# Optimization experiments

Measured on AMD Instinct MI355X. Metric: run time of the kernel, lower is better.

## Reference

```python
import jax, jax.numpy as jnp
import numpy as np

B, S, H, R, NH = 4, 2048, 1024, 512, 8
HD = R // NH
EPS = 1e-5


def _ln(x, g, b):
    m = jnp.mean(x, axis=-1, keepdims=True)
    v = jnp.mean(jnp.square(x - m), axis=-1, keepdims=True)
    return (x - m) * jax.lax.rsqrt(v + EPS) * g + b


def setup_inputs() -> dict:
    key = jax.random.key(0)
    ks = iter(jax.random.split(key, 40))
    s = 0.02
    d = {}
    d['hidden_states'] = jax.random.normal(next(ks), (B, S, H), dtype=jnp.float32)
    # complexity assessor: H -> H//4 -> 32 -> 1
    d['ca_w1'] = jax.random.normal(next(ks), (H, H // 4)) * s
    d['ca_b1'] = jnp.zeros((H // 4,))
    d['ca_w2'] = jax.random.normal(next(ks), (H // 4, 32)) * s
    d['ca_b2'] = jnp.zeros((32,))
    d['ca_w3'] = jax.random.normal(next(ks), (32, 1)) * s
    d['ca_b3'] = jnp.zeros((1,))
    # reasoning projection H -> R, and pre-norm
    d['rp_w'] = jax.random.normal(next(ks), (H, R)) * s
    d['rp_b'] = jnp.zeros((R,))
    d['rn_g'] = jnp.ones((R,)); d['rn_b'] = jnp.zeros((R,))
    # transformer encoder layer (norm_first)
    d['ln1_g'] = jnp.ones((R,)); d['ln1_b'] = jnp.zeros((R,))
    d['wqkv'] = jax.random.normal(next(ks), (R, 3 * R)) * s
    d['bqkv'] = jnp.zeros((3 * R,))
    d['wo'] = jax.random.normal(next(ks), (R, R)) * s
    d['bo'] = jnp.zeros((R,))
    d['ln2_g'] = jnp.ones((R,)); d['ln2_b'] = jnp.zeros((R,))
    d['ff1_w'] = jax.random.normal(next(ks), (R, 4 * R)) * s
    d['ff1_b'] = jnp.zeros((4 * R,))
    d['ff2_w'] = jax.random.normal(next(ks), (4 * R, R)) * s
    d['ff2_b'] = jnp.zeros((R,))
    # output projection R -> H and norm
    d['op_w'] = jax.random.normal(next(ks), (R, H)) * s
    d['op_b'] = jnp.zeros((H,))
    d['on_g'] = jnp.ones((H,)); d['on_b'] = jnp.zeros((H,))
    # integration gate: 2H -> H -> H
    d['gw1'] = jax.random.normal(next(ks), (2 * H, H)) * s
    d['gb1'] = jnp.zeros((H,))
    d['gw2'] = jax.random.normal(next(ks), (H, H)) * s
    d['gb2'] = jnp.zeros((H,))
    return d


def reference(hidden_states, ca_w1, ca_b1, ca_w2, ca_b2, ca_w3, ca_b3,
              rp_w, rp_b, rn_g, rn_b, ln1_g, ln1_b, wqkv, bqkv, wo, bo,
              ln2_g, ln2_b, ff1_w, ff1_b, ff2_w, ff2_b, op_w, op_b,
              on_g, on_b, gw1, gb1, gw2, gb2):
    # complexity assessment (metrics only; input_ids=None forces reasoning on all)
    pooled = jnp.mean(hidden_states, axis=1)  # [B,H]
    h = jax.nn.relu(pooled @ ca_w1 + ca_b1)
    h = jax.nn.relu(h @ ca_w2 + ca_b2)
    complexity_scores = jax.nn.sigmoid(h @ ca_w3 + ca_b3)[:, 0]  # [B]

    # apply_reasoning on full batch (should_reason is all-True)
    r = _ln(hidden_states @ rp_w + rp_b, rn_g, rn_b)  # [B,S,R]

    # TransformerEncoderLayer, norm_first, relu, dropout=0
    y = _ln(r, ln1_g, ln1_b)
    qkv = y @ wqkv + bqkv
    q, k, v = jnp.split(qkv, 3, axis=-1)
    q = q.reshape(B, S, NH, HD)
    k = k.reshape(B, S, NH, HD)
    v = v.reshape(B, S, NH, HD)
    scores = jnp.einsum('bqhd,bkhd->bhqk', q, k) / np.sqrt(HD).astype(np.float32)
    attn = jax.nn.softmax(scores, axis=-1)
    o = jnp.einsum('bhqk,bkhd->bqhd', attn, v).reshape(B, S, R)
    r = r + (o @ wo + bo)
    y = _ln(r, ln2_g, ln2_b)
    r = r + (jax.nn.relu(y @ ff1_w + ff1_b) @ ff2_w + ff2_b)

    reasoned = _ln(r @ op_w + op_b, on_g, on_b)  # [B,S,H]

    # sigmoid integration gate on concat([states, reasoned])
    gate_in = jnp.concatenate([hidden_states, reasoned], axis=-1)
    g = jax.nn.relu(gate_in @ gw1 + gb1)
    g = jax.nn.sigmoid(g @ gw2 + gb2)
    output = hidden_states + g * reasoned
    return output, complexity_scores
```

## Files before the change

### kernel.cpp

```cpp
#include <hip/hip_runtime.h>
#include <hip/hip_bf16.h>
#include <math.h>


typedef __bf16 bf16;
typedef __attribute__((ext_vector_type(8))) __bf16 bf16x8;
typedef __attribute__((ext_vector_type(4))) float f32x4;
typedef __attribute__((ext_vector_type(16))) float f32x16;

__device__ __forceinline__ void glds16(const bf16* g, bf16* l) {
  __builtin_amdgcn_global_load_lds(
      (const __attribute__((address_space(1))) void*)g,
      (__attribute__((address_space(3))) void*)l, 16, 0, 0);
}

struct TD { const float* src; char* dst; int rows, cols, tx, start, outbf; };
struct TDs { TD d[9]; };
__global__ void k_trans_all(TDs td) {
  int bid = blockIdx.x;
  int si = 0;
  for (int i = 1; i < 9; i++)
    if (bid >= td.d[i].start) si = i;
  TD dd = td.d[si];
  int tid = bid - dd.start;
  int bx = tid % dd.tx, by = tid / dd.tx;
  __shared__ float tile[32][33];
  int c0 = bx * 32, r0 = by * 32;
  int tx = threadIdx.x, ty = threadIdx.y;
  for (int i = 0; i < 32; i += 8)
    tile[ty + i][tx] = dd.src[(long)(r0 + ty + i) * dd.cols + (c0 + tx)];
  __syncthreads();
  if (dd.outbf) {
    bf16* o = (bf16*)dd.dst;
    for (int i = 0; i < 32; i += 8)
      o[(long)(c0 + ty + i) * dd.rows + (r0 + tx)] = (bf16)tile[tx][ty + i];
  } else {
    float* o = (float*)dd.dst;
    for (int i = 0; i < 32; i += 8)
      o[(long)(c0 + ty + i) * dd.rows + (r0 + tx)] = tile[tx][ty + i];
  }
}

__global__ void k_cvt(const float* __restrict__ in, bf16* __restrict__ out) {
  long i = ((long)blockIdx.x * 256 + threadIdx.x) * 4;
  float4 v = *(const float4*)(in + i);
  bf16* o = out + i;
  o[0] = (bf16)v.x; o[1] = (bf16)v.y; o[2] = (bf16)v.z; o[3] = (bf16)v.w;
}

__global__ void k_vtrans(const bf16* __restrict__ qkv, bf16* __restrict__ VT) {
  __shared__ bf16 tile[32][33];
  int bh = blockIdx.z, b = bh >> 3, h = bh & 7;
  const bf16* in = qkv + (long)b * 2048 * 1536 + 1024 + h * 64;
  bf16* out = VT + (long)bh * 64 * 2048;
  int c0 = blockIdx.x * 32, r0 = blockIdx.y * 32;
  int tx = threadIdx.x, ty = threadIdx.y;
  for (int i = 0; i < 32; i += 8)
    tile[ty + i][tx] = in[(long)(r0 + ty + i) * 1536 + (c0 + tx)];
  __syncthreads();
  for (int i = 0; i < 32; i += 8)
    out[(long)(c0 + ty + i) * 2048 + (r0 + tx)] = tile[tx][ty + i];
}

__global__ void k_pool_part(const float* __restrict__ X, float* __restrict__ part) {
  int b = blockIdx.y, c = blockIdx.z;
  int col = blockIdx.x * 256 + threadIdx.x;
  const float* p = X + (long)b * 2048 * 1024 + (long)c * 128 * 1024 + col;
  float s = 0.f;
  for (int i = 0; i < 128; i++) s += p[(long)i * 1024];
  part[((long)c * 4 + b) * 1024 + col] = s;
}

__global__ void k_pool_fin(const float* __restrict__ part, float* __restrict__ pooled) {
  int idx = blockIdx.x * 256 + threadIdx.x;
  int b = idx >> 10, col = idx & 1023;
  float s = 0.f;
  for (int c = 0; c < 16; c++) s += part[((long)c * 4 + b) * 1024 + col];
  pooled[idx] = s * (1.0f / 2048.0f);
}

__global__ void k_ca1(const float* __restrict__ pooled, const float* __restrict__ w1T,
                      const float* __restrict__ b1, float* __restrict__ h1) {
  int t = blockIdx.x, b = threadIdx.x >> 6, lane = threadIdx.x & 63;
  const float* wr = w1T + (long)t * 1024 + lane * 16;
  const float* pr = pooled + b * 1024 + lane * 16;
  float acc = 0.f;
  for (int j = 0; j < 4; j++) {
    float4 w = *(const float4*)(wr + j * 4);
    float4 p = *(const float4*)(pr + j * 4);
    acc += w.x * p.x + w.y * p.y + w.z * p.z + w.w * p.w;
  }
  for (int off = 32; off; off >>= 1) acc += __shfl_xor(acc, off);
  if (lane == 0) h1[b * 256 + t] = fmaxf(acc + b1[t], 0.f);
}

__global__ void k_ca2(const float* __restrict__ h1,
                      const float* __restrict__ w2, const float* __restrict__ b2,
                      const float* __restrict__ w3, const float* __restrict__ b3,
                      float* __restrict__ scores) {
  __shared__ float w2s[256 * 32];
  __shared__ float h1s[4 * 256];
  __shared__ float h2s[4][32];
  int t = threadIdx.x;
  for (int j = 0; j < 32; j++) w2s[j * 256 + t] = w2[j * 256 + t];
  for (int j = 0; j < 4; j++) h1s[j * 256 + t] = h1[j * 256 + t];
  __syncthreads();
  if (t < 128) {
    int b = t >> 5, o = t & 31;
    float acc = b2[o];
    for (int k = 0; k < 256; k++) acc += h1s[b * 256 + k] * w2s[k * 32 + o];
    h2s[b][o] = fmaxf(acc, 0.f);
  }
  __syncthreads();
  if (t < 4) {
    float acc = b3[0];
    for (int k = 0; k < 32; k++) acc += h2s[t][k] * w3[k];
    scores[t] = 1.f / (1.f + expf(-acc));
  }
}

template <int NCOL>
__global__ void k_ln(const bf16* __restrict__ in, const float* __restrict__ g,
                     const float* __restrict__ be, bf16* __restrict__ out) {
  int wave = threadIdx.x >> 6, lane = threadIdx.x & 63;
  long row = (long)blockIdx.x * 4 + wave;
  const bf16* x = in + row * NCOL;
  constexpr int PER = NCOL / 64;
  constexpr int CH = PER / 8;
  float v[PER];
  float s = 0.f;
  for (int c = 0; c < CH; c++) {
    bf16x8 t = *(const bf16x8*)(x + c * 512 + lane * 8);
    for (int j = 0; j < 8; j++) { v[c * 8 + j] = (float)t[j]; s += v[c * 8 + j]; }
  }
  for (int off = 32; off; off >>= 1) s += __shfl_xor(s, off);
  float mean = s * (1.0f / NCOL);
  float q = 0.f;
  for (int i = 0; i < PER; i++) { float d = v[i] - mean; q += d * d; }
  for (int off = 32; off; off >>= 1) q += __shfl_xor(q, off);
  float rstd = rsqrtf(q * (1.0f / NCOL) + 1e-5f);
  for (int c = 0; c < CH; c++) {
    bf16x8 o;
    for (int j = 0; j < 8; j++) {
      int col = c * 512 + lane * 8 + j;
      o[j] = (bf16)((v[c * 8 + j] - mean) * rstd * g[col] + be[col]);
    }
    *(bf16x8*)(out + row * NCOL + c * 512 + lane * 8) = o;
  }
}

__global__ void k_ln2(const bf16* __restrict__ in,
                      const float* __restrict__ g1, const float* __restrict__ b1,
                      const float* __restrict__ g2, const float* __restrict__ b2,
                      bf16* __restrict__ outR, bf16* __restrict__ outY) {
  int wave = threadIdx.x >> 6, lane = threadIdx.x & 63;
  long row = (long)blockIdx.x * 4 + wave;
  const bf16* x = in + row * 512;
  float v[8];
  float s = 0.f;
  bf16x8 t = *(const bf16x8*)(x + lane * 8);
  for (int j = 0; j < 8; j++) { v[j] = (float)t[j]; s += v[j]; }
  for (int off = 32; off; off >>= 1) s += __shfl_xor(s, off);
  float mean = s * (1.0f / 512);
  float q = 0.f;
  for (int j = 0; j < 8; j++) { float d = v[j] - mean; q += d * d; }
  for (int off = 32; off; off >>= 1) q += __shfl_xor(q, off);
  float rstd = rsqrtf(q * (1.0f / 512) + 1e-5f);
  float r[8];
  float s2 = 0.f;
  bf16x8 orr;
  for (int j = 0; j < 8; j++) {
    int col = lane * 8 + j;
    r[j] = (v[j] - mean) * rstd * g1[col] + b1[col];
    orr[j] = (bf16)r[j];
    s2 += r[j];
  }
  *(bf16x8*)(outR + row * 512 + lane * 8) = orr;
  for (int off = 32; off; off >>= 1) s2 += __shfl_xor(s2, off);
  float mean2 = s2 * (1.0f / 512);
  float q2 = 0.f;
  for (int j = 0; j < 8; j++) { float d = r[j] - mean2; q2 += d * d; }
  for (int off = 32; off; off >>= 1) q2 += __shfl_xor(q2, off);
  float rstd2 = rsqrtf(q2 * (1.0f / 512) + 1e-5f);
  bf16x8 oy;
  for (int j = 0; j < 8; j++) {
    int col = lane * 8 + j;
    oy[j] = (bf16)((r[j] - mean2) * rstd2 * g2[col] + b2[col]);
  }
  *(bf16x8*)(outY + row * 512 + lane * 8) = oy;
}

template <int EPI, int MT>
__launch_bounds__(256, 2)
__global__ void k_gemm(const bf16* __restrict__ A1, int ldA1,
                       const bf16* __restrict__ B1, int ldB1, int K1,
                       const bf16* __restrict__ A2, int ldA2,
                       const bf16* __restrict__ B2, int ldB2, int K2,
                       const float* __restrict__ bias, void* __restrict__ out,
                       int ldOut, const bf16* __restrict__ resid, int ldRes,
                       const float* __restrict__ auxX, const bf16* __restrict__ auxR) {
  __shared__ __align__(16) bf16 As[MT * 32];
  __shared__ __align__(16) bf16 Bs[128 * 32];
  constexpr int NF = (MT == 128) ? 4 : 2;
  constexpr int NW = (MT == 128) ? 64 : 32;
  int t = threadIdx.x;
  int wave = t >> 6, lane = t & 63, quad = lane >> 4, l16 = lane & 15;
  int wy = (MT == 128) ? (wave >> 1) : 0;
  int wx = (MT == 128) ? (wave & 1) : wave;
  int m0 = blockIdx.y * MT, n0 = blockIdx.x * 128;
  int sr = t >> 2;
  int sc = (t & 3) * 8;
  bf16* la0 = As + wave * 512;
  bf16* la1 = As + 2048 + wave * 512;
  bf16* lb0 = Bs + wave * 512;
  bf16* lb1 = Bs + 2048 + wave * 512;

  f32x4 acc[4][NF] = {};

  auto run = [&](const bf16* A, int ldA, const bf16* Bt, int ldB, int K) {
    const bf16* ag0 = A + (long)(m0 + sr) * ldA + sc;
    const bf16* ag1 = ag0 + (long)64 * ldA;
    const bf16* bg0 = Bt + (long)(n0 + sr) * ldB + sc;
    const bf16* bg1 = bg0 + (long)64 * ldB;
    for (int kt = 0; kt < K; kt += 32) {
      glds16(ag0 + kt, la0);
      if constexpr (MT == 128) glds16(ag1 + kt, la1);
      glds16(bg0 + kt, lb0);
      glds16(bg1 + kt, lb1);
      __syncthreads();
      bf16x8 af[4], bfr[NF];
      for (int im = 0; im < 4; im++)
        af[im] = *(const bf16x8*)(As + (64 * wy + 16 * im + l16) * 32 + quad * 8);
      for (int in = 0; in < NF; in++)
        bfr[in] = *(const bf16x8*)(Bs + (NW * wx + 16 * in + l16) * 32 + quad * 8);
      for (int im = 0; im < 4; im++)
        for (int in = 0; in < NF; in++)
          acc[im][in] = __builtin_amdgcn_mfma_f32_16x16x32_bf16(af[im], bfr[in],
                                                                acc[im][in], 0, 0, 0);
      __syncthreads();
    }
  };
  run(A1, ldA1, B1, ldB1, K1);
  if (A2) run(A2, ldA2, B2, ldB2, K2);

  int rb = m0 + 64 * wy + quad * 4;
  int cb = n0 + NW * wx + l16;
  for (int im = 0; im < 4; im++)
    for (int in = 0; in < NF; in++)
      for (int i = 0; i < 4; i++) {
        int row = rb + 16 * im + i;
        int col = cb + 16 * in;
        long o = (long)row * ldOut + col;
        float v = acc[im][in][i] + bias[col];
        if constexpr (EPI == 0) ((bf16*)out)[o] = (bf16)v;
        else if constexpr (EPI == 1) ((bf16*)out)[o] = (bf16)fmaxf(v, 0.f);
        else if constexpr (EPI == 2)
          ((bf16*)out)[o] = (bf16)(v + (float)resid[(long)row * ldRes + col]);
        else {
          float gg = 1.f / (1.f + expf(-v));
          ((float*)out)[o] = auxX[o] + gg * (float)auxR[o];
        }
      }
}

__launch_bounds__(256, 4)
__global__ void k_attn(const bf16* __restrict__ qkv, const bf16* __restrict__ VT,
                       bf16* __restrict__ Op0, bf16* __restrict__ Op1,
                       float* __restrict__ lp) {
  __shared__ __align__(16) bf16 Ks[64 * 72];
  __shared__ __align__(16) bf16 Vs[64 * 72];
  __shared__ __align__(16) bf16 PQs[128 * 72];
  int t = threadIdx.x, wave = t >> 6, lane = t & 63;
  int l32 = lane & 31, half = lane >> 5;
  int q0 = blockIdx.x * 128;
  int h = blockIdx.y >> 1, split = blockIdx.y & 1, b = blockIdx.z;
  const bf16* qb = qkv + (long)b * 2048 * 1536 + h * 64;
  const bf16* vb = VT + (long)(b * 8 + h) * 64 * 2048;
  bf16* Op = split ? Op1 : Op0;

  for (int i = 0; i < 4; i++) {
    int idx = i * 256 + t, q = idx >> 3, cg = idx & 7;
    *(uint4*)(PQs + q * 72 + cg * 8) =
        *(const uint4*)(qb + (long)(q0 + q) * 1536 + cg * 8);
  }
  __syncthreads();
  bf16x8 qf[4];
  for (int c = 0; c < 4; c++)
    qf[c] = *(const bf16x8*)(PQs + (wave * 32 + l32) * 72 + c * 16 + half * 8);

  float rs[16];
  for (int i = 0; i < 16; i++) rs[i] = 0.f;
  f32x16 oacc[2] = {};
  const float scale = 0.125f;

  for (int kt = split * 16; kt < split * 16 + 16; kt++) {
    int k0 = kt * 64;
    __syncthreads();
    for (int i = 0; i < 2; i++) {
      int idx = i * 256 + t, r = idx >> 3, cg = idx & 7;
      *(uint4*)(Ks + r * 72 + cg * 8) =
          *(const uint4*)(qb + 512 + (long)(k0 + r) * 1536 + cg * 8);
      *(uint4*)(Vs + r * 72 + cg * 8) =
          *(const uint4*)(vb + (long)r * 2048 + k0 + cg * 8);
    }
    __syncthreads();

    for (int kb = 0; kb < 2; kb++) {
      f32x16 s = {};
      for (int c = 0; c < 4; c++) {
        bf16x8 kf = *(const bf16x8*)(Ks + (kb * 32 + l32) * 72 + c * 16 + half * 8);
        s = __builtin_amdgcn_mfma_f32_32x32x16_bf16(qf[c], kf, s, 0, 0, 0);
      }
      for (int r = 0; r < 16; r++) {
        float p = __expf(s[r] * scale);
        rs[r] += p;
        int row = (r & 3) + 8 * (r >> 2) + 4 * half;
        PQs[(wave * 32 + row) * 72 + kb * 32 + l32] = (bf16)p;
      }
    }
    for (int c = 0; c < 4; c++) {
      bf16x8 pf = *(const bf16x8*)(PQs + (wave * 32 + l32) * 72 + c * 16 + half * 8);
      for (int db = 0; db < 2; db++) {
        bf16x8 vf = *(const bf16x8*)(Vs + (db * 32 + l32) * 72 + c * 16 + half * 8);
        oacc[db] = __builtin_amdgcn_mfma_f32_32x32x16_bf16(pf, vf, oacc[db], 0, 0, 0);
      }
    }
  }
  for (int r = 0; r < 16; r++)
    for (int off = 1; off < 32; off <<= 1) rs[r] += __shfl_xor(rs[r], off);
  for (int r = 0; r < 16; r++) {
    float inv = 1.f / rs[r];
    int row = q0 + wave * 32 + (r & 3) + 8 * (r >> 2) + 4 * half;
    long grow = (long)b * 2048 + row;
    long gr = grow * 512 + h * 64;
    Op[gr + l32] = (bf16)(oacc[0][r] * inv);
    Op[gr + 32 + l32] = (bf16)(oacc[1][r] * inv);
    if (l32 == 0) lp[(split << 16) + grow * 8 + h] = rs[r];
  }
}

__global__ void k_attn_fin(const bf16* __restrict__ O0, const bf16* __restrict__ O1,
                           const float* __restrict__ lp, bf16* __restrict__ out) {
  long idx = (long)blockIdx.x * 256 + threadIdx.x;
  long row = idx >> 6;
  int c8 = (int)(idx & 63);
  int h = c8 >> 3;
  float l0 = lp[row * 8 + h], l1 = lp[65536 + row * 8 + h];
  float inv = 1.f / (l0 + l1);
  float w0 = l0 * inv, w1 = l1 * inv;
  bf16x8 a = *(const bf16x8*)(O0 + idx * 8);
  bf16x8 bb = *(const bf16x8*)(O1 + idx * 8);
  bf16x8 o;
  for (int j = 0; j < 8; j++) o[j] = (bf16)((float)a[j] * w0 + (float)bb[j] * w1);
  *(bf16x8*)(out + idx * 8) = o;
}

extern "C" void kernel_launch(void* const* d_in, const int* in_sizes, int n_in,
                              void* d_out, int out_size, void* d_ws, size_t ws_size,
                              hipStream_t stream) {
  const float* X    = (const float*)d_in[0];
  const float* caw1 = (const float*)d_in[1];
  const float* cab1 = (const float*)d_in[2];
  const float* caw2 = (const float*)d_in[3];
  const float* cab2 = (const float*)d_in[4];
  const float* caw3 = (const float*)d_in[5];
  const float* cab3 = (const float*)d_in[6];
  const float* rp_w = (const float*)d_in[7];
  const float* rp_b = (const float*)d_in[8];
  const float* rn_g = (const float*)d_in[9];
  const float* rn_b = (const float*)d_in[10];
  const float* ln1g = (const float*)d_in[11];
  const float* ln1b = (const float*)d_in[12];
  const float* wqkv = (const float*)d_in[13];
  const float* bqkv = (const float*)d_in[14];
  const float* wo   = (const float*)d_in[15];
  const float* bo   = (const float*)d_in[16];
  const float* ln2g = (const float*)d_in[17];
  const float* ln2b = (const float*)d_in[18];
  const float* ff1w = (const float*)d_in[19];
  const float* ff1b = (const float*)d_in[20];
  const float* ff2w = (const float*)d_in[21];
  const float* ff2b = (const float*)d_in[22];
  const float* opw  = (const float*)d_in[23];
  const float* opb  = (const float*)d_in[24];
  const float* ong  = (const float*)d_in[25];
  const float* onb  = (const float*)d_in[26];
  const float* gw1  = (const float*)d_in[27];
  const float* gb1  = (const float*)d_in[28];
  const float* gw2  = (const float*)d_in[29];
  const float* gb2  = (const float*)d_in[30];

  char* ws = (char*)d_ws;
  const size_t MB = 1u << 20;
  const size_t KB = 1u << 10;
  bf16* rpwT  = (bf16*)ws;
  bf16* wqkvT = rpwT + 524288;
  bf16* woT   = wqkvT + 786432;
  bf16* ff1T  = woT + 262144;
  bf16* ff2T  = ff1T + 1048576;
  bf16* opT   = ff2T + 1048576;
  bf16* gw1T  = opT + 524288;
  bf16* gw2T  = gw1T + 2097152;
  float* part   = (float*)(ws + 14 * MB);
  float* lpart  = (float*)(ws + 14 * MB);
  float* pooled = (float*)(ws + 14 * MB + 512 * KB);
  float* h1buf  = (float*)(ws + 14 * MB + 528 * KB);
  bf16* Xb   = (bf16*)(ws + 15 * MB);
  bf16* bufA = (bf16*)(ws + 31 * MB);
  bf16* bufB = (bf16*)(ws + 39 * MB);
  bf16* bufC = (bf16*)(ws + 47 * MB);
  bf16* qkv  = (bf16*)(ws + 55 * MB);
  float* w1T = (float*)(ws + 55 * MB);
  bf16* VT   = (bf16*)(ws + 79 * MB);
  bf16* f1   = (bf16*)(ws + 55 * MB);
  bf16* tmp3 = (bf16*)(ws + 55 * MB);
  bf16* rsn  = (bf16*)(ws + 71 * MB);
  bf16* g1   = (bf16*)(ws + 31 * MB);

  TDs td;
  td.d[0] = {rp_w, (char*)rpwT, 1024, 512, 16, 0, 1};
  td.d[1] = {wqkv, (char*)wqkvT, 512, 1536, 48, 512, 1};
  td.d[2] = {wo, (char*)woT, 512, 512, 16, 1280, 1};
  td.d[3] = {ff1w, (char*)ff1T, 512, 2048, 64, 1536, 1};
  td.d[4] = {ff2w, (char*)ff2T, 2048, 512, 16, 2560, 1};
  td.d[5] = {opw, (char*)opT, 512, 1024, 32, 3584, 1};
  td.d[6] = {gw1, (char*)gw1T, 2048, 1024, 32, 4096, 1};
  td.d[7] = {gw2, (char*)gw2T, 1024, 1024, 32, 6144, 1};
  td.d[8] = {caw1, (char*)w1T, 1024, 256, 8, 7168, 0};
  dim3 b32x8(32, 8);
  k_trans_all<<<7424, b32x8, 0, stream>>>(td);
  k_cvt<<<8192, 256, 0, stream>>>(X, Xb);

  k_pool_part<<<dim3(4, 4, 16), 256, 0, stream>>>(X, part);
  k_pool_fin<<<16, 256, 0, stream>>>(part, pooled);
  k_ca1<<<256, 256, 0, stream>>>(pooled, w1T, cab1, h1buf);
  k_ca2<<<1, 256, 0, stream>>>(h1buf, caw2, cab2, caw3, cab3,
                               (float*)d_out + 8388608);

  k_gemm<0, 64><<<dim3(4, 128), 256, 0, stream>>>(
      Xb, 1024, rpwT, 1024, 1024, nullptr, 0, nullptr, 0, 0,
      rp_b, bufA, 512, nullptr, 0, nullptr, nullptr);
  k_ln2<<<2048, 256, 0, stream>>>(bufA, rn_g, rn_b, ln1g, ln1b, bufB, bufC);
  k_gemm<0, 128><<<dim3(12, 64), 256, 0, stream>>>(
      bufC, 512, wqkvT, 512, 512, nullptr, 0, nullptr, 0, 0,
      bqkv, qkv, 1536, nullptr, 0, nullptr, nullptr);
  k_vtrans<<<dim3(2, 64, 32), b32x8, 0, stream>>>(qkv, VT);
  k_attn<<<dim3(16, 16, 4), 256, 0, stream>>>(qkv, VT, bufA, bufC, lpart);
  k_attn_fin<<<2048, 256, 0, stream>>>(bufA, bufC, lpart, bufC);
  k_gemm<2, 64><<<dim3(4, 128), 256, 0, stream>>>(
      bufC, 512, woT, 512, 512, nullptr, 0, nullptr, 0, 0,
      bo, bufA, 512, bufB, 512, nullptr, nullptr);
  k_ln<512><<<2048, 256, 0, stream>>>(bufA, ln2g, ln2b, bufB);
  k_gemm<1, 128><<<dim3(16, 64), 256, 0, stream>>>(
      bufB, 512, ff1T, 512, 512, nullptr, 0, nullptr, 0, 0,
      ff1b, f1, 2048, nullptr, 0, nullptr, nullptr);
  k_gemm<2, 64><<<dim3(4, 128), 256, 0, stream>>>(
      f1, 2048, ff2T, 2048, 2048, nullptr, 0, nullptr, 0, 0,
      ff2b, bufC, 512, bufA, 512, nullptr, nullptr);
  k_gemm<0, 128><<<dim3(8, 64), 256, 0, stream>>>(
      bufC, 512, opT, 512, 512, nullptr, 0, nullptr, 0, 0,
      opb, tmp3, 1024, nullptr, 0, nullptr, nullptr);
  k_ln<1024><<<2048, 256, 0, stream>>>(tmp3, ong, onb, rsn);
  k_gemm<1, 128><<<dim3(8, 64), 256, 0, stream>>>(
      Xb, 1024, gw1T, 2048, 1024, rsn, 1024, gw1T + 1024, 2048, 1024,
      gb1, g1, 1024, nullptr, 0, nullptr, nullptr);
  k_gemm<5, 128><<<dim3(8, 64), 256, 0, stream>>>(
      g1, 1024, gw2T, 1024, 1024, nullptr, 0, nullptr, 0, 0,
      gb2, (float*)d_out, 1024, nullptr, 0, X, rsn);
}
```

Before: 487.7 us.

## Split attention KV range three ways, shrink LDS, fold X conversion into transpose kernel

Attention now splits the key range into three parts instead of two (11/11/10 tiles), writing the third partial output into the V columns of the qkv buffer, which are no longer needed after V was transposed. The P staging buffer shrinks to a 32-wide per-kb tile and the Q preload reuses the K/V buffer, cutting LDS so occupancy can rise to 5 blocks per CU. The finish kernel merges three partials. The fp32-to-bf16 conversion of X moves into the batched transpose kernel as a new mode, removing one launch. The trade-off is more partial-output traffic and a third read in the merge step.

```diff
diff --git a/kernel.cpp b/kernel.cpp
--- a/kernel.cpp
+++ b/kernel.cpp
@@ -14,23 +14,31 @@
       (__attribute__((address_space(3))) void*)l, 16, 0, 0);
 }
 
-struct TD { const float* src; char* dst; int rows, cols, tx, start, outbf; };
-struct TDs { TD d[9]; };
+struct TD { const float* src; char* dst; int rows, cols, tx, start, mode; };
+struct TDs { TD d[10]; };
 __global__ void k_trans_all(TDs td) {
   int bid = blockIdx.x;
   int si = 0;
-  for (int i = 1; i < 9; i++)
+  for (int i = 1; i < 10; i++)
     if (bid >= td.d[i].start) si = i;
   TD dd = td.d[si];
   int tid = bid - dd.start;
   int bx = tid % dd.tx, by = tid / dd.tx;
-  __shared__ float tile[32][33];
   int c0 = bx * 32, r0 = by * 32;
   int tx = threadIdx.x, ty = threadIdx.y;
+  if (dd.mode == 2) {
+    bf16* o = (bf16*)dd.dst;
+    for (int i = 0; i < 32; i += 8) {
+      long idx = (long)(r0 + ty + i) * dd.cols + (c0 + tx);
+      o[idx] = (bf16)dd.src[idx];
+    }
+    return;
+  }
+  __shared__ float tile[32][33];
   for (int i = 0; i < 32; i += 8)
     tile[ty + i][tx] = dd.src[(long)(r0 + ty + i) * dd.cols + (c0 + tx)];
   __syncthreads();
-  if (dd.outbf) {
+  if (dd.mode == 0) {
     bf16* o = (bf16*)dd.dst;
     for (int i = 0; i < 32; i += 8)
       o[(long)(c0 + ty + i) * dd.rows + (r0 + tx)] = (bf16)tile[tx][ty + i];
@@ -39,13 +47,6 @@
     for (int i = 0; i < 32; i += 8)
       o[(long)(c0 + ty + i) * dd.rows + (r0 + tx)] = tile[tx][ty + i];
   }
-}
-
-__global__ void k_cvt(const float* __restrict__ in, bf16* __restrict__ out) {
-  long i = ((long)blockIdx.x * 256 + threadIdx.x) * 4;
-  float4 v = *(const float4*)(in + i);
-  bf16* o = out + i;
-  o[0] = (bf16)v.x; o[1] = (bf16)v.y; o[2] = (bf16)v.z; o[3] = (bf16)v.w;
 }
 
 __global__ void k_vtrans(const bf16* __restrict__ qkv, bf16* __restrict__ VT) {
@@ -263,37 +264,41 @@
       }
 }
 
-__launch_bounds__(256, 4)
-__global__ void k_attn(const bf16* __restrict__ qkv, const bf16* __restrict__ VT,
+__launch_bounds__(256, 5)
+__global__ void k_attn(const bf16* qkv, const bf16* __restrict__ VT,
                        bf16* __restrict__ Op0, bf16* __restrict__ Op1,
-                       float* __restrict__ lp) {
-  __shared__ __align__(16) bf16 Ks[64 * 72];
-  __shared__ __align__(16) bf16 Vs[64 * 72];
-  __shared__ __align__(16) bf16 PQs[128 * 72];
+                       bf16* qkvV, float* __restrict__ lp) {
+  __shared__ __align__(16) bf16 KVs[2 * 64 * 72];
+  __shared__ __align__(16) bf16 Ps[128 * 40];
+  bf16* Ks = KVs;
+  bf16* Vs = KVs + 64 * 72;
   int t = threadIdx.x, wave = t >> 6, lane = t & 63;
   int l32 = lane & 31, half = lane >> 5;
   int q0 = blockIdx.x * 128;
-  int h = blockIdx.y >> 1, split = blockIdx.y & 1, b = blockIdx.z;
+  int h = blockIdx.y / 3, split = blockIdx.y % 3, b = blockIdx.z;
   const bf16* qb = qkv + (long)b * 2048 * 1536 + h * 64;
   const bf16* vb = VT + (long)(b * 8 + h) * 64 * 2048;
-  bf16* Op = split ? Op1 : Op0;
+  bf16* Op = (split == 0) ? Op0 : (split == 1) ? Op1 : qkvV;
+  long ldO = (split == 2) ? 1536 : 512;
 
   for (int i = 0; i < 4; i++) {
     int idx = i * 256 + t, q = idx >> 3, cg = idx & 7;
-    *(uint4*)(PQs + q * 72 + cg * 8) =
+    *(uint4*)(KVs + q * 64 + cg * 8) =
         *(const uint4*)(qb + (long)(q0 + q) * 1536 + cg * 8);
   }
   __syncthreads();
   bf16x8 qf[4];
   for (int c = 0; c < 4; c++)
-    qf[c] = *(const bf16x8*)(PQs + (wave * 32 + l32) * 72 + c * 16 + half * 8);
+    qf[c] = *(const bf16x8*)(KVs + (wave * 32 + l32) * 64 + c * 16 + half * 8);
 
   float rs[16];
   for (int i = 0; i < 16; i++) rs[i] = 0.f;
   f32x16 oacc[2] = {};
   const float scale = 0.125f;
 
-  for (int kt = split * 16; kt < split * 16 + 16; kt++) {
+  int kt0 = split * 11;
+  int kt1 = (split == 2) ? 32 : kt0 + 11;
+  for (int kt = kt0; kt < kt1; kt++) {
     int k0 = kt * 64;
     __syncthreads();
     for (int i = 0; i < 2; i++) {
@@ -315,14 +320,15 @@
         float p = __expf(s[r] * scale);
         rs[r] += p;
         int row = (r & 3) + 8 * (r >> 2) + 4 * half;
-        PQs[(wave * 32 + row) * 72 + kb * 32 + l32] = (bf16)p;
+        Ps[(wave * 32 + row) * 40 + l32] = (bf16)p;
       }
-    }
-    for (int c = 0; c < 4; c++) {
-      bf16x8 pf = *(const bf16x8*)(PQs + (wave * 32 + l32) * 72 + c * 16 + half * 8);
-      for (int db = 0; db < 2; db++) {
-        bf16x8 vf = *(const bf16x8*)(Vs + (db * 32 + l32) * 72 + c * 16 + half * 8);
-        oacc[db] = __builtin_amdgcn_mfma_f32_32x32x16_bf16(pf, vf, oacc[db], 0, 0, 0);
+      for (int c2 = 0; c2 < 2; c2++) {
+        bf16x8 pf = *(const bf16x8*)(Ps + (wave * 32 + l32) * 40 + c2 * 16 + half * 8);
+        for (int db = 0; db < 2; db++) {
+          bf16x8 vf = *(const bf16x8*)(Vs + (db * 32 + l32) * 72 +
+                                       kb * 32 + c2 * 16 + half * 8);
+          oacc[db] = __builtin_amdgcn_mfma_f32_32x32x16_bf16(pf, vf, oacc[db], 0, 0, 0);
+        }
       }
     }
   }
@@ -332,26 +338,30 @@
     float inv = 1.f / rs[r];
     int row = q0 + wave * 32 + (r & 3) + 8 * (r >> 2) + 4 * half;
     long grow = (long)b * 2048 + row;
-    long gr = grow * 512 + h * 64;
+    long gr = grow * ldO + h * 64;
     Op[gr + l32] = (bf16)(oacc[0][r] * inv);
     Op[gr + 32 + l32] = (bf16)(oacc[1][r] * inv);
-    if (l32 == 0) lp[(split << 16) + grow * 8 + h] = rs[r];
+    if (l32 == 0) lp[split * 65536 + grow * 8 + h] = rs[r];
   }
 }
 
 __global__ void k_attn_fin(const bf16* __restrict__ O0, const bf16* __restrict__ O1,
+                           const bf16* __restrict__ O2 ,
                            const float* __restrict__ lp, bf16* __restrict__ out) {
   long idx = (long)blockIdx.x * 256 + threadIdx.x;
   long row = idx >> 6;
   int c8 = (int)(idx & 63);
   int h = c8 >> 3;
-  float l0 = lp[row * 8 + h], l1 = lp[65536 + row * 8 + h];
-  float inv = 1.f / (l0 + l1);
-  float w0 = l0 * inv, w1 = l1 * inv;
+  float l0 = lp[row * 8 + h];
+  float l1 = lp[65536 + row * 8 + h];
+  float l2 = lp[131072 + row * 8 + h];
+  float inv = 1.f / (l0 + l1 + l2);
   bf16x8 a = *(const bf16x8*)(O0 + idx * 8);
   bf16x8 bb = *(const bf16x8*)(O1 + idx * 8);
+  bf16x8 cc = *(const bf16x8*)(O2 + row * 1536 + c8 * 8);
   bf16x8 o;
-  for (int j = 0; j < 8; j++) o[j] = (bf16)((float)a[j] * w0 + (float)bb[j] * w1);
+  for (int j = 0; j < 8; j++)
+    o[j] = (bf16)(((float)a[j] * l0 + (float)bb[j] * l1 + (float)cc[j] * l2) * inv);
   *(bf16x8*)(out + idx * 8) = o;
 }
 
@@ -402,9 +412,9 @@
   bf16* gw1T  = opT + 524288;
   bf16* gw2T  = gw1T + 2097152;
   float* part   = (float*)(ws + 14 * MB);
-  float* lpart  = (float*)(ws + 14 * MB);
   float* pooled = (float*)(ws + 14 * MB + 512 * KB);
   float* h1buf  = (float*)(ws + 14 * MB + 528 * KB);
+  float* lpart  = (float*)(ws + 14 * MB);
   bf16* Xb   = (bf16*)(ws + 15 * MB);
   bf16* bufA = (bf16*)(ws + 31 * MB);
   bf16* bufB = (bf16*)(ws + 39 * MB);
@@ -418,18 +428,18 @@
   bf16* g1   = (bf16*)(ws + 31 * MB);
 
   TDs td;
-  td.d[0] = {rp_w, (char*)rpwT, 1024, 512, 16, 0, 1};
-  td.d[1] = {wqkv, (char*)wqkvT, 512, 1536, 48, 512, 1};
-  td.d[2] = {wo, (char*)woT, 512, 512, 16, 1280, 1};
-  td.d[3] = {ff1w, (char*)ff1T, 512, 2048, 64, 1536, 1};
-  td.d[4] = {ff2w, (char*)ff2T, 2048, 512, 16, 2560, 1};
-  td.d[5] = {opw, (char*)opT, 512, 1024, 32, 3584, 1};
-  td.d[6] = {gw1, (char*)gw1T, 2048, 1024, 32, 4096, 1};
-  td.d[7] = {gw2, (char*)gw2T, 1024, 1024, 32, 6144, 1};
-  td.d[8] = {caw1, (char*)w1T, 1024, 256, 8, 7168, 0};
+  td.d[0] = {rp_w, (char*)rpwT, 1024, 512, 16, 0, 0};
+  td.d[1] = {wqkv, (char*)wqkvT, 512, 1536, 48, 512, 0};
+  td.d[2] = {wo, (char*)woT, 512, 512, 16, 1280, 0};
+  td.d[3] = {ff1w, (char*)ff1T, 512, 2048, 64, 1536, 0};
+  td.d[4] = {ff2w, (char*)ff2T, 2048, 512, 16, 2560, 0};
+  td.d[5] = {opw, (char*)opT, 512, 1024, 32, 3584, 0};
+  td.d[6] = {gw1, (char*)gw1T, 2048, 1024, 32, 4096, 0};
+  td.d[7] = {gw2, (char*)gw2T, 1024, 1024, 32, 6144, 0};
+  td.d[8] = {caw1, (char*)w1T, 1024, 256, 8, 7168, 1};
+  td.d[9] = {X, (char*)Xb, 8192, 1024, 32, 7424, 2};
   dim3 b32x8(32, 8);
-  k_trans_all<<<7424, b32x8, 0, stream>>>(td);
-  k_cvt<<<8192, 256, 0, stream>>>(X, Xb);
+  k_trans_all<<<15616, b32x8, 0, stream>>>(td);
 
   k_pool_part<<<dim3(4, 4, 16), 256, 0, stream>>>(X, part);
   k_pool_fin<<<16, 256, 0, stream>>>(part, pooled);
@@ -445,8 +455,9 @@
       bufC, 512, wqkvT, 512, 512, nullptr, 0, nullptr, 0, 0,
       bqkv, qkv, 1536, nullptr, 0, nullptr, nullptr);
   k_vtrans<<<dim3(2, 64, 32), b32x8, 0, stream>>>(qkv, VT);
-  k_attn<<<dim3(16, 16, 4), 256, 0, stream>>>(qkv, VT, bufA, bufC, lpart);
-  k_attn_fin<<<2048, 256, 0, stream>>>(bufA, bufC, lpart, bufC);
+  k_attn<<<dim3(16, 24, 4), 256, 0, stream>>>(qkv, VT, bufA, bufC,
+                                              qkv + 1024, lpart);
+  k_attn_fin<<<2048, 256, 0, stream>>>(bufA, bufC, qkv + 1024, lpart, bufC);
   k_gemm<2, 64><<<dim3(4, 128), 256, 0, stream>>>(
       bufC, 512, woT, 512, 512, nullptr, 0, nullptr, 0, 0,
       bo, bufA, 512, bufB, 512, nullptr, nullptr);
```

New measurement: 577.4 us. 1.18x slower.
